# Kernel optimization log

Hardware: AMD Instinct MI355X
Metric: run time of the kernel (lower is better)

The kernel has to match this reference:

```python
import jax, jax.numpy as jnp
import numpy as np

D_MODEL = 1024
N_HEADS = 16
D_KV = 64
ROPE_THETA = 10000.0


def setup_inputs() -> dict:
    key = jax.random.key(0)
    k1, k2, k3, k4, k5 = jax.random.split(key, 5)
    B, S = 4, 2048
    scale = 0.02
    return {
        "positions": jnp.arange(S, dtype=jnp.int64 if jax.config.jax_enable_x64 else jnp.int32),
        "hidden_states": jax.random.normal(k1, (B, S, D_MODEL), dtype=jnp.float32),
        "wq": jax.random.normal(k2, (D_MODEL, N_HEADS * D_KV), dtype=jnp.float32) * scale,
        "wk": jax.random.normal(k3, (D_MODEL, N_HEADS * D_KV), dtype=jnp.float32) * scale,
        "wv": jax.random.normal(k4, (D_MODEL, N_HEADS * D_KV), dtype=jnp.float32) * scale,
        "wo": jax.random.normal(k5, (N_HEADS * D_KV, D_MODEL), dtype=jnp.float32) * scale,
    }


def _rope(positions, q, k):
    # Neox-style simple RoPE, matching SimpleRoPE fallback.
    # q, k: [B, H, S, Dh]
    Dh = q.shape[-1]
    inv_freq = 1.0 / (ROPE_THETA ** (jnp.arange(0, Dh, 2, dtype=jnp.float32) / Dh))  # [Dh/2]
    freqs = positions.astype(jnp.float32)[:, None] * inv_freq[None, :]  # [S, Dh/2]
    emb = jnp.concatenate([freqs, freqs], axis=-1)  # [S, Dh]
    cos = jnp.cos(emb)[None, None, :, :]
    sin = jnp.sin(emb)[None, None, :, :]

    def rotate_half(x):
        x1, x2 = jnp.split(x, 2, axis=-1)
        return jnp.concatenate([-x2, x1], axis=-1)

    q_rot = q * cos + rotate_half(q) * sin
    k_rot = k * cos + rotate_half(k) * sin
    return q_rot, k_rot


def reference(positions, hidden_states, wq, wk, wv, wo):
    B, S, _ = hidden_states.shape
    H, Dh = N_HEADS, D_KV

    def split_heads(x):  # [B, S, H*Dh] -> [B, H, S, Dh]
        return x.reshape(B, S, H, Dh).transpose(0, 2, 1, 3)

    q = split_heads(hidden_states @ wq)
    k = split_heads(hidden_states @ wk)
    v = split_heads(hidden_states @ wv)

    q, k = _rope(positions, q, k)

    # scale = 1.0 (no 1/sqrt(d) scaling), matching the source module
    scores = jnp.einsum("bhqd,bhkd->bhqk", q, k)
    attn = jax.nn.softmax(scores.astype(jnp.float32), axis=-1).astype(scores.dtype)
    # dropout is identity in eval mode
    out = jnp.einsum("bhqk,bhkd->bhqd", attn, v)  # [B, H, S, Dh]
    out = out.transpose(0, 2, 1, 3).reshape(B, S, H * Dh)
    return out @ wo
```

## Files before the change

### kernel.cpp

```cpp
#include <hip/hip_runtime.h>
#include <hip/hip_bf16.h>


typedef __bf16 bf16_t;
typedef __bf16 bf16x4 __attribute__((ext_vector_type(4)));
typedef __bf16 bf16x8 __attribute__((ext_vector_type(8)));
typedef float f32x4 __attribute__((ext_vector_type(4)));

#define MFMA16(a, b, c) __builtin_amdgcn_mfma_f32_16x16x32_bf16((a), (b), (c), 0, 0, 0)

#define GLOAD_LDS(gp, lp) \
  __builtin_amdgcn_global_load_lds( \
      (const __attribute__((address_space(1))) void*)(gp), \
      (__attribute__((address_space(3))) void*)(lp), 16, 0, 0)

__global__ __launch_bounds__(256) void cvt_kernel(const float* __restrict__ X,
                                                  bf16_t* __restrict__ Y) {
  const int i = (blockIdx.x * 256 + threadIdx.x) * 4;
  const f32x4 x = *(const f32x4*)(X + i);
  bf16x4 y;
#pragma unroll
  for (int k = 0; k < 4; k++) y[k] = (bf16_t)x[k];
  *(bf16x4*)(Y + i) = y;
}

__global__ __launch_bounds__(256) void wtrans4_kernel(
    const float* __restrict__ w0, const float* __restrict__ w1,
    const float* __restrict__ w2, const float* __restrict__ w3,
    bf16_t* __restrict__ out) {
  __shared__ bf16_t t[32][33];
  const int tx = threadIdx.x, ty = threadIdx.y;
  const int bx = blockIdx.x, by = blockIdx.y, z = blockIdx.z;
  const float* W = (z == 0) ? w0 : (z == 1) ? w1 : (z == 2) ? w2 : w3;
  bf16_t* Wt = out + (size_t)z * 1024 * 1024;
#pragma unroll
  for (int i = ty; i < 32; i += 8)
    t[i][tx] = (bf16_t)W[(size_t)(by * 32 + i) * 1024 + bx * 32 + tx];
  __syncthreads();
#pragma unroll
  for (int i = ty; i < 32; i += 8)
    Wt[(size_t)(bx * 32 + i) * 1024 + by * 32 + tx] = t[tx][i];
}

__global__ __launch_bounds__(256) void vtrans_kernel(const bf16_t* __restrict__ V,
                                                     bf16_t* __restrict__ VT) {
  __shared__ bf16_t t[32][33];
  const int tx = threadIdx.x, ty = threadIdx.y;
  const int sx = blockIdx.x * 32, cy = blockIdx.y * 32, b = blockIdx.z;
  const bf16_t* Vb = V + (size_t)b * 2048 * 1024;
  bf16_t* VTb = VT + (size_t)b * 1024 * 2048;
#pragma unroll
  for (int i = ty; i < 32; i += 8)
    t[i][tx] = Vb[(size_t)(sx + i) * 1024 + cy + tx];
  __syncthreads();
#pragma unroll
  for (int i = ty; i < 32; i += 8)
    VTb[(size_t)(cy + i) * 2048 + sx + tx] = t[tx][i];
}

template <typename TC, bool FUSED_QKV>
__global__ __launch_bounds__(256) void gemm_kernel(
    const bf16_t* __restrict__ A, const bf16_t* __restrict__ BtBase,
    TC* __restrict__ CBase, const int ropeIn) {
  constexpr int K = 1024, N = 1024;
  __shared__ __align__(16) bf16_t As[128 * 32];
  __shared__ __align__(16) bf16_t Bs[128 * 32];

  const int tid = threadIdx.x;
  const int lane = tid & 63, w = tid >> 6;
  const int l15 = lane & 15, quad = lane >> 4;
  const int wm = w >> 1, wn = w & 1;
  const int m0 = blockIdx.x * 128;

  int n0, rope;
  const bf16_t* Bt;
  TC* C;
  if (FUSED_QKV) {
    const int which = blockIdx.y >> 3;
    n0 = (blockIdx.y & 7) * 128;
    Bt = BtBase + (size_t)which * (1u << 20);
    C = CBase + (size_t)which * (8u << 20);
    rope = (which < 2);
  } else {
    n0 = blockIdx.y * 128;
    Bt = BtBase;
    C = CBase;
    rope = ropeIn;
  }

  f32x4 acc[4][4] = {};
  const int li8 = lane >> 3, j = lane & 7;

  for (int k0 = 0; k0 < K; k0 += 32) {
#pragma unroll
    for (int p = 0; p < 2; ++p) {
      const int g = w * 16 + p * 8 + li8;
      const int jp = j ^ (g & 7);
      const int row = 2 * g + (jp >> 2), kb = jp & 3;
      GLOAD_LDS(A + (size_t)(m0 + row) * K + k0 + kb * 8, As + (w * 16 + p * 8) * 64);
      GLOAD_LDS(Bt + (size_t)(n0 + row) * K + k0 + kb * 8, Bs + (w * 16 + p * 8) * 64);
    }
    __syncthreads();

    bf16x8 af[4], bfv[4];
#pragma unroll
    for (int mi = 0; mi < 4; mi++) {
      const int R = wm * 64 + mi * 16 + l15, g = R >> 1;
      const int jj = (((R & 1) << 2) | quad) ^ (g & 7);
      af[mi] = *(const bf16x8*)(As + g * 64 + jj * 8);
    }
#pragma unroll
    for (int ni = 0; ni < 4; ni++) {
      const int R = wn * 64 + ni * 16 + l15, g = R >> 1;
      const int jj = (((R & 1) << 2) | quad) ^ (g & 7);
      bfv[ni] = *(const bf16x8*)(Bs + g * 64 + jj * 8);
    }
#pragma unroll
    for (int mi = 0; mi < 4; mi++)
#pragma unroll
      for (int ni = 0; ni < 4; ni++)
        acc[mi][ni] = MFMA16(af[mi], bfv[ni], acc[mi][ni]);
    __syncthreads();
  }

#pragma unroll
  for (int mi = 0; mi < 4; mi++) {
    const int rbase = m0 + wm * 64 + mi * 16 + quad * 4;
    if (rope) {
#pragma unroll
      for (int r = 0; r < 4; r++) {
        const float pos = (float)((rbase + r) & 2047);
#pragma unroll
        for (int ni = 0; ni < 2; ni++) {
          const int d2 = ni * 16 + l15;
          const float invf = __powf(10000.0f, -(float)d2 * (1.0f / 32.0f));
          float sv, cv;
          __sincosf(pos * invf, &sv, &cv);
          const float a0 = acc[mi][ni][r], a2 = acc[mi][ni + 2][r];
          acc[mi][ni][r] = a0 * cv - a2 * sv;
          acc[mi][ni + 2][r] = a2 * cv + a0 * sv;
        }
      }
    }
#pragma unroll
    for (int ni = 0; ni < 4; ni++) {
      const int c0 = n0 + wn * 64 + ni * 16 + l15;
#pragma unroll
      for (int r = 0; r < 4; r++)
        C[(size_t)(rbase + r) * N + c0] = (TC)acc[mi][ni][r];
    }
  }
}

#define PSTR 48

__global__ __launch_bounds__(256) void attn_kernel(const bf16_t* __restrict__ Q,
                                                   const bf16_t* __restrict__ K,
                                                   const bf16_t* __restrict__ VT,
                                                   bf16_t* __restrict__ O) {
  __shared__ __align__(16) bf16_t Kl[2][64 * 64];
  __shared__ __align__(16) bf16_t Vl[2][64 * 64];
  __shared__ __align__(16) bf16_t Pl[4 * 16 * PSTR];

  const int tid = threadIdx.x;
  const int lane = tid & 63, wv = tid >> 6;
  const int l15 = lane & 15, quad = lane >> 4;

  const int orig = blockIdx.y * 32 + blockIdx.x;
  const int wk = (orig & 7) * 256 + (orig >> 3);
  const int q0 = (wk & 31) * 64;
  const int bh = wk >> 5, b = bh >> 4, h = bh & 15;

  const size_t base = (size_t)b * 2048 * 1024 + (size_t)h * 64;
  const bf16_t* Qb = Q + base;
  const bf16_t* Kb = K + base;
  const bf16_t* VTb = VT + (size_t)(b * 1024 + h * 64) * 2048;

  const int qrow = q0 + wv * 16 + l15;
  bf16x8 qf[2];
  qf[0] = *(const bf16x8*)(Qb + (size_t)qrow * 1024 + quad * 8);
  qf[1] = *(const bf16x8*)(Qb + (size_t)qrow * 1024 + 32 + quad * 8);

  f32x4 accO[4] = {};
  float lsum[4] = {0.f, 0.f, 0.f, 0.f};

  const int li8 = lane >> 3, j = lane & 7;

  auto stage = [&](int buf, int kvb) {
#pragma unroll
    for (int p = 0; p < 2; ++p) {
      const int kr = wv * 16 + p * 8 + li8;
      const int blk = j ^ (kr & 7);
      GLOAD_LDS(Kb + (size_t)(kvb + kr) * 1024 + blk * 8, &Kl[buf][(wv * 16 + p * 8) * 64]);
      GLOAD_LDS(VTb + (size_t)kr * 2048 + kvb + blk * 8, &Vl[buf][(wv * 16 + p * 8) * 64]);
    }
  };

  stage(0, 0);
  for (int t = 0; t < 32; ++t) {
    const int cur = t & 1;
    if (t < 31) {
      stage(cur ^ 1, (t + 1) * 64);
      __asm__ volatile("s_waitcnt vmcnt(4)" ::: "memory");
    } else {
      __asm__ volatile("s_waitcnt vmcnt(0)" ::: "memory");
    }
    __builtin_amdgcn_s_barrier();

    f32x4 sc[4] = {};
    __builtin_amdgcn_s_setprio(1);
#pragma unroll
    for (int tt = 0; tt < 2; tt++)
#pragma unroll
      for (int nb = 0; nb < 4; nb++) {
        const int R = nb * 16 + l15;
        const int jj = (tt * 4 + quad) ^ (R & 7);
        const bf16x8 kf = *(const bf16x8*)(&Kl[cur][R * 64 + jj * 8]);
        sc[nb] = MFMA16(qf[tt], kf, sc[nb]);
      }
    __builtin_amdgcn_s_setprio(0);

#pragma unroll
    for (int hf = 0; hf < 2; hf++) {
#pragma unroll
      for (int nb2 = 0; nb2 < 2; nb2++)
#pragma unroll
        for (int r = 0; r < 4; r++) {
          const float p = __expf(sc[hf * 2 + nb2][r]);
          lsum[r] += p;
          Pl[wv * 16 * PSTR + (quad * 4 + r) * PSTR + nb2 * 16 + l15] = (bf16_t)p;
        }
      __asm__ volatile("s_waitcnt lgkmcnt(0)" ::: "memory");
      const bf16x8 pf = *(const bf16x8*)(&Pl[wv * 16 * PSTR + l15 * PSTR + quad * 8]);
      __builtin_amdgcn_s_setprio(1);
#pragma unroll
      for (int nb = 0; nb < 4; nb++) {
        const int R = nb * 16 + l15;
        const int jj = (hf * 4 + quad) ^ (R & 7);
        const bf16x8 vf = *(const bf16x8*)(&Vl[cur][R * 64 + jj * 8]);
        accO[nb] = MFMA16(pf, vf, accO[nb]);
      }
      __builtin_amdgcn_s_setprio(0);
    }
    __builtin_amdgcn_s_barrier();
  }

#pragma unroll
  for (int r = 0; r < 4; r++) {
    float s = lsum[r];
    s += __shfl_xor(s, 1);
    s += __shfl_xor(s, 2);
    s += __shfl_xor(s, 4);
    s += __shfl_xor(s, 8);
    lsum[r] = 1.0f / s;
  }
  bf16_t* Ob = O + base;
#pragma unroll
  for (int r = 0; r < 4; r++) {
    const int qr = q0 + wv * 16 + quad * 4 + r;
#pragma unroll
    for (int nb = 0; nb < 4; nb++)
      Ob[(size_t)qr * 1024 + nb * 16 + l15] = (bf16_t)(accO[nb][r] * lsum[r]);
  }
}

extern "C" void kernel_launch(void* const* d_in, const int* in_sizes, int n_in,
                              void* d_out, int out_size, void* d_ws, size_t ws_size,
                              hipStream_t stream) {
  const float* hs = (const float*)d_in[1];
  const float* wq = (const float*)d_in[2];
  const float* wk = (const float*)d_in[3];
  const float* wv = (const float*)d_in[4];
  const float* wo = (const float*)d_in[5];

  char* ws = (char*)d_ws;
  const size_t MB = 1024 * 1024;
  bf16_t* WtQKV = (bf16_t*)(ws + 0 * MB);
  bf16_t* WtO = (bf16_t*)(ws + 6 * MB);
  bf16_t* hsb = (bf16_t*)(ws + 8 * MB);
  bf16_t* VT = (bf16_t*)(ws + 8 * MB);
  bf16_t* Qw = (bf16_t*)(ws + 24 * MB);
  bf16_t* Kw = (bf16_t*)(ws + 40 * MB);
  bf16_t* Vw = (bf16_t*)(ws + 56 * MB);
  bf16_t* Ow = (bf16_t*)(ws + 56 * MB);

  wtrans4_kernel<<<dim3(32, 32, 4), dim3(32, 8), 0, stream>>>(wq, wk, wv, wo, WtQKV);
  cvt_kernel<<<8192, 256, 0, stream>>>(hs, hsb);

  gemm_kernel<bf16_t, true><<<dim3(64, 24), 256, 0, stream>>>(hsb, WtQKV, Qw, 0);

  vtrans_kernel<<<dim3(64, 32, 4), dim3(32, 8), 0, stream>>>(Vw, VT);

  attn_kernel<<<dim3(32, 64), 256, 0, stream>>>(Qw, Kw, VT, Ow);

  gemm_kernel<float, false><<<dim3(64, 8), 256, 0, stream>>>(Ow, WtO, (float*)d_out, 0);
}
```

Baseline: 341.3 us.

## Rewrite attention with 32x32 MFMA, register-resident P, and 128-row query tiles

The attention kernel now computes the transposed score tile (K·Q^T) with 32x32x16 MFMAs. Each wave owns 32 query rows, so a block covers 128 queries, which halves the grid and doubles reuse of each staged K/V tile. The exp'd probabilities are packed to bf16 and rearranged across lane halves with shuffles into the B operand of the PV MFMA, removing the LDS round trip for P. Output is staged through LDS for coalesced 16-byte stores. Risks include higher register pressure from two f32x16 accumulators, a per-iteration full __syncthreads, and a grid of 1024 blocks that may fill the CUs less well.

```diff
diff --git a/kernel.cpp b/kernel.cpp
--- a/kernel.cpp
+++ b/kernel.cpp
@@ -3,16 +3,27 @@
 
 
 typedef __bf16 bf16_t;
+typedef __bf16 bf16x2 __attribute__((ext_vector_type(2)));
 typedef __bf16 bf16x4 __attribute__((ext_vector_type(4)));
 typedef __bf16 bf16x8 __attribute__((ext_vector_type(8)));
 typedef float f32x4 __attribute__((ext_vector_type(4)));
+typedef float f32x16 __attribute__((ext_vector_type(16)));
+typedef unsigned u32x4 __attribute__((ext_vector_type(4)));
 
 #define MFMA16(a, b, c) __builtin_amdgcn_mfma_f32_16x16x32_bf16((a), (b), (c), 0, 0, 0)
+#define MFMA32(a, b, c) __builtin_amdgcn_mfma_f32_32x32x16_bf16((a), (b), (c), 0, 0, 0)
 
 #define GLOAD_LDS(gp, lp) \
   __builtin_amdgcn_global_load_lds( \
       (const __attribute__((address_space(1))) void*)(gp), \
       (__attribute__((address_space(3))) void*)(lp), 16, 0, 0)
+
+static __device__ __forceinline__ unsigned pk2(float a, float b) {
+  bf16x2 t;
+  t[0] = (bf16_t)a;
+  t[1] = (bf16_t)b;
+  return __builtin_bit_cast(unsigned, t);
+}
 
 __global__ __launch_bounds__(256) void cvt_kernel(const float* __restrict__ X,
                                                   bf16_t* __restrict__ Y) {
@@ -152,39 +163,37 @@
   }
 }
 
-#define PSTR 48
-
 __global__ __launch_bounds__(256) void attn_kernel(const bf16_t* __restrict__ Q,
                                                    const bf16_t* __restrict__ K,
                                                    const bf16_t* __restrict__ VT,
                                                    bf16_t* __restrict__ O) {
   __shared__ __align__(16) bf16_t Kl[2][64 * 64];
   __shared__ __align__(16) bf16_t Vl[2][64 * 64];
-  __shared__ __align__(16) bf16_t Pl[4 * 16 * PSTR];
+  __shared__ __align__(16) bf16_t Ot[4][32 * 72];
 
   const int tid = threadIdx.x;
   const int lane = tid & 63, wv = tid >> 6;
-  const int l15 = lane & 15, quad = lane >> 4;
-
-  const int orig = blockIdx.y * 32 + blockIdx.x;
-  const int wk = (orig & 7) * 256 + (orig >> 3);
-  const int q0 = (wk & 31) * 64;
-  const int bh = wk >> 5, b = bh >> 4, h = bh & 15;
+  const int l31 = lane & 31, hi = lane >> 5;
+  const int li8 = lane >> 3, j = lane & 7;
+
+  const int orig = blockIdx.y * 16 + blockIdx.x;
+  const int wk = (orig & 7) * 128 + (orig >> 3);
+  const int q0 = (wk & 15) * 128;
+  const int bh = wk >> 4, b = bh >> 4, h = bh & 15;
 
   const size_t base = (size_t)b * 2048 * 1024 + (size_t)h * 64;
   const bf16_t* Qb = Q + base;
   const bf16_t* Kb = K + base;
   const bf16_t* VTb = VT + (size_t)(b * 1024 + h * 64) * 2048;
 
-  const int qrow = q0 + wv * 16 + l15;
-  bf16x8 qf[2];
-  qf[0] = *(const bf16x8*)(Qb + (size_t)qrow * 1024 + quad * 8);
-  qf[1] = *(const bf16x8*)(Qb + (size_t)qrow * 1024 + 32 + quad * 8);
-
-  f32x4 accO[4] = {};
-  float lsum[4] = {0.f, 0.f, 0.f, 0.f};
-
-  const int li8 = lane >> 3, j = lane & 7;
+  const int qrow = q0 + wv * 32 + l31;
+  bf16x8 qf[4];
+#pragma unroll
+  for (int kk = 0; kk < 4; kk++)
+    qf[kk] = *(const bf16x8*)(Qb + (size_t)qrow * 1024 + kk * 16 + hi * 8);
+
+  f32x16 accO0 = {}, accO1 = {};
+  float ls0 = 0.f, ls1 = 0.f, ls2 = 0.f, ls3 = 0.f;
 
   auto stage = [&](int buf, int kvb) {
 #pragma unroll
@@ -197,70 +206,107 @@
   };
 
   stage(0, 0);
+  __syncthreads();
+
   for (int t = 0; t < 32; ++t) {
     const int cur = t & 1;
-    if (t < 31) {
-      stage(cur ^ 1, (t + 1) * 64);
-      __asm__ volatile("s_waitcnt vmcnt(4)" ::: "memory");
-    } else {
-      __asm__ volatile("s_waitcnt vmcnt(0)" ::: "memory");
-    }
-    __builtin_amdgcn_s_barrier();
-
-    f32x4 sc[4] = {};
-    __builtin_amdgcn_s_setprio(1);
-#pragma unroll
-    for (int tt = 0; tt < 2; tt++)
-#pragma unroll
-      for (int nb = 0; nb < 4; nb++) {
-        const int R = nb * 16 + l15;
-        const int jj = (tt * 4 + quad) ^ (R & 7);
+    if (t < 31) stage(cur ^ 1, (t + 1) * 64);
+
+#pragma unroll
+    for (int s = 0; s < 2; ++s) {
+      f32x16 st = {};
+#pragma unroll
+      for (int kk = 0; kk < 4; kk++) {
+        const int R = s * 32 + l31;
+        const int jj = (kk * 2 + hi) ^ (R & 7);
         const bf16x8 kf = *(const bf16x8*)(&Kl[cur][R * 64 + jj * 8]);
-        sc[nb] = MFMA16(qf[tt], kf, sc[nb]);
-      }
-    __builtin_amdgcn_s_setprio(0);
-
-#pragma unroll
-    for (int hf = 0; hf < 2; hf++) {
-#pragma unroll
-      for (int nb2 = 0; nb2 < 2; nb2++)
-#pragma unroll
-        for (int r = 0; r < 4; r++) {
-          const float p = __expf(sc[hf * 2 + nb2][r]);
-          lsum[r] += p;
-          Pl[wv * 16 * PSTR + (quad * 4 + r) * PSTR + nb2 * 16 + l15] = (bf16_t)p;
+        st = MFMA32(kf, qf[kk], st);
+      }
+
+      unsigned Aw0, Aw1, Aw2, Aw3, Bw0, Bw1, Bw2, Bw3;
+      {
+        float p0, p1, p2, p3;
+        p0 = __expf(st[0]);  p1 = __expf(st[1]);
+        p2 = __expf(st[2]);  p3 = __expf(st[3]);
+        ls0 += p0; ls1 += p1; ls2 += p2; ls3 += p3;
+        Aw0 = pk2(p0, p1); Bw0 = pk2(p2, p3);
+        p0 = __expf(st[4]);  p1 = __expf(st[5]);
+        p2 = __expf(st[6]);  p3 = __expf(st[7]);
+        ls0 += p0; ls1 += p1; ls2 += p2; ls3 += p3;
+        Aw1 = pk2(p0, p1); Bw1 = pk2(p2, p3);
+        p0 = __expf(st[8]);  p1 = __expf(st[9]);
+        p2 = __expf(st[10]); p3 = __expf(st[11]);
+        ls0 += p0; ls1 += p1; ls2 += p2; ls3 += p3;
+        Aw2 = pk2(p0, p1); Bw2 = pk2(p2, p3);
+        p0 = __expf(st[12]); p1 = __expf(st[13]);
+        p2 = __expf(st[14]); p3 = __expf(st[15]);
+        ls0 += p0; ls1 += p1; ls2 += p2; ls3 += p3;
+        Aw3 = pk2(p0, p1); Bw3 = pk2(p2, p3);
+      }
+
+      {
+        const unsigned ax0 = (unsigned)__shfl_xor((int)Aw0, 32);
+        const unsigned ax1 = (unsigned)__shfl_xor((int)Aw1, 32);
+        const unsigned bx0 = (unsigned)__shfl_xor((int)Bw0, 32);
+        const unsigned bx1 = (unsigned)__shfl_xor((int)Bw1, 32);
+        const unsigned ax2 = (unsigned)__shfl_xor((int)Aw2, 32);
+        const unsigned ax3 = (unsigned)__shfl_xor((int)Aw3, 32);
+        const unsigned bx2 = (unsigned)__shfl_xor((int)Bw2, 32);
+        const unsigned bx3 = (unsigned)__shfl_xor((int)Bw3, 32);
+        const bool hiH = hi != 0;
+        const unsigned nA0 = hiH ? ax1 : Aw0, nA1 = hiH ? Aw1 : ax0;
+        const unsigned nB0 = hiH ? bx1 : Bw0, nB1 = hiH ? Bw1 : bx0;
+        const unsigned nA2 = hiH ? ax3 : Aw2, nA3 = hiH ? Aw3 : ax2;
+        const unsigned nB2 = hiH ? bx3 : Bw2, nB3 = hiH ? Bw3 : bx2;
+        Aw0 = nA0; Aw1 = nA1; Bw0 = nB0; Bw1 = nB1;
+        Aw2 = nA2; Aw3 = nA3; Bw2 = nB2; Bw3 = nB3;
+      }
+      const u32x4 f0w = {Aw0, Bw0, Aw1, Bw1};
+      const u32x4 f1w = {Aw2, Bw2, Aw3, Bw3};
+      const bf16x8 f0 = __builtin_bit_cast(bf16x8, f0w);
+      const bf16x8 f1 = __builtin_bit_cast(bf16x8, f1w);
+
+#pragma unroll
+      for (int t2 = 0; t2 < 2; ++t2) {
+        const bf16x8 pb = t2 ? f1 : f0;
+        const int tkv = s * 2 + t2;
+#pragma unroll
+        for (int ds = 0; ds < 2; ++ds) {
+          const int R = ds * 32 + l31;
+          const int jj = (tkv * 2 + hi) ^ (R & 7);
+          const bf16x8 vf = *(const bf16x8*)(&Vl[cur][R * 64 + jj * 8]);
+          if (ds == 0)
+            accO0 = MFMA32(vf, pb, accO0);
+          else
+            accO1 = MFMA32(vf, pb, accO1);
         }
-      __asm__ volatile("s_waitcnt lgkmcnt(0)" ::: "memory");
-      const bf16x8 pf = *(const bf16x8*)(&Pl[wv * 16 * PSTR + l15 * PSTR + quad * 8]);
-      __builtin_amdgcn_s_setprio(1);
-#pragma unroll
-      for (int nb = 0; nb < 4; nb++) {
-        const int R = nb * 16 + l15;
-        const int jj = (hf * 4 + quad) ^ (R & 7);
-        const bf16x8 vf = *(const bf16x8*)(&Vl[cur][R * 64 + jj * 8]);
-        accO[nb] = MFMA16(pf, vf, accO[nb]);
-      }
-      __builtin_amdgcn_s_setprio(0);
-    }
-    __builtin_amdgcn_s_barrier();
-  }
-
-#pragma unroll
-  for (int r = 0; r < 4; r++) {
-    float s = lsum[r];
-    s += __shfl_xor(s, 1);
-    s += __shfl_xor(s, 2);
-    s += __shfl_xor(s, 4);
-    s += __shfl_xor(s, 8);
-    lsum[r] = 1.0f / s;
-  }
-  bf16_t* Ob = O + base;
-#pragma unroll
-  for (int r = 0; r < 4; r++) {
-    const int qr = q0 + wv * 16 + quad * 4 + r;
-#pragma unroll
-    for (int nb = 0; nb < 4; nb++)
-      Ob[(size_t)qr * 1024 + nb * 16 + l15] = (bf16_t)(accO[nb][r] * lsum[r]);
+      }
+    }
+    __syncthreads();
+  }
+
+  float ls = (ls0 + ls1) + (ls2 + ls3);
+  ls += __shfl_xor(ls, 32);
+  const float inv = 1.0f / ls;
+
+  bf16_t* const ot = &Ot[wv][0];
+#pragma unroll
+  for (int ds = 0; ds < 2; ++ds) {
+    const f32x16 ac = ds ? accO1 : accO0;
+#pragma unroll
+    for (int g = 0; g < 4; ++g) {
+      const int d0 = ds * 32 + g * 8 + hi * 4;
+      *(unsigned*)(ot + l31 * 72 + d0) = pk2(ac[g * 4 + 0] * inv, ac[g * 4 + 1] * inv);
+      *(unsigned*)(ot + l31 * 72 + d0 + 2) = pk2(ac[g * 4 + 2] * inv, ac[g * 4 + 3] * inv);
+    }
+  }
+  __syncthreads();
+  bf16_t* const Ob = O + base;
+#pragma unroll
+  for (int i = 0; i < 4; ++i) {
+    const int qq = i * 8 + li8;
+    const bf16x8 vv = *(const bf16x8*)(ot + qq * 72 + j * 8);
+    *(bf16x8*)(Ob + (size_t)(q0 + wv * 32 + qq) * 1024 + j * 8) = vv;
   }
 }
 
@@ -291,7 +337,7 @@
 
   vtrans_kernel<<<dim3(64, 32, 4), dim3(32, 8), 0, stream>>>(Vw, VT);
 
-  attn_kernel<<<dim3(32, 64), 256, 0, stream>>>(Qw, Kw, VT, Ow);
+  attn_kernel<<<dim3(16, 64), 256, 0, stream>>>(Qw, Kw, VT, Ow);
 
   gemm_kernel<float, false><<<dim3(64, 8), 256, 0, stream>>>(Ow, WtO, (float*)d_out, 0);
 }
```

Result: faster. 333.5 us (-2.3%).
